# Kernel tuning notes

Measured on AMD Instinct MI355X. Metric: run time of the kernel, lower is better.

## Reference

```python
import jax, jax.numpy as jnp
import numpy as np

D_MODEL = 768
HIDDEN = 2048  # round(768*8/3)=2048, already a multiple of 64
N_EXPERTS = 8
ALPHA = 0.05  # load_balance_alpha


def setup_inputs() -> dict:
    key = jax.random.key(0)
    k0, k1, k2, k3, k4 = jax.random.split(key, 5)
    x = jax.random.normal(k0, (2, 2048, D_MODEL), dtype=jnp.float32)
    wg_w = jax.random.normal(k1, (N_EXPERTS, D_MODEL), dtype=jnp.float32) * 0.02
    wg_b = jnp.zeros((N_EXPERTS,), dtype=jnp.float32)
    Wu = jax.random.normal(k2, (N_EXPERTS, D_MODEL, HIDDEN), dtype=jnp.float32) * 0.02
    Wv = jax.random.normal(k3, (N_EXPERTS, D_MODEL, HIDDEN), dtype=jnp.float32) * 0.02
    Wd = jax.random.normal(k4, (N_EXPERTS, HIDDEN, D_MODEL), dtype=jnp.float32) * 0.02
    return {"x": x, "wg_w": wg_w, "wg_b": wg_b, "Wu": Wu, "Wv": Wv, "Wd": Wd}


def reference(x, wg_w, wg_b, Wu, Wv, Wd):
    b, t, d = x.shape
    xf = x.reshape(b * t, d)  # [N, d]

    # ---- Top1Router (eval mode: temp=1, no noise, z_loss_coef=0) ----
    logits = xf @ wg_w.T + wg_b            # [N, E]
    probs = jax.nn.softmax(logits, axis=-1)
    top1_idx = jnp.argmax(logits, axis=-1)  # [N]
    top1_p = jnp.take_along_axis(probs, top1_idx[:, None], axis=1)[:, 0]  # [N]

    # aux loss: me and ce computed under no_grad in the torch source -> stop_gradient
    one_hot = jax.nn.one_hot(top1_idx, N_EXPERTS, dtype=probs.dtype)
    me = jax.lax.stop_gradient(one_hot.mean(axis=0))   # [E]
    ce = jax.lax.stop_gradient(probs.mean(axis=0))     # [E]
    aux = ALPHA * N_EXPERTS * jnp.sum(me * ce)

    # ---- Dropless dispatch: per-expert masked SwiGLU, combined with top1 gate ----
    gate = top1_p[:, None]  # [N, 1]
    y = jnp.zeros_like(xf)
    for e in range(N_EXPERTS):
        mask = (top1_idx == e)[:, None]            # [N, 1]
        xe = jnp.where(mask, xf, 0.0)              # zero-out non-routed tokens (no biases -> exact)
        u = xe @ Wu[e]                              # [N, H]
        v = xe @ Wv[e]                              # [N, H]
        ye = (jax.nn.silu(u) * v) @ Wd[e]           # [N, d]
        y = y + jnp.where(mask, ye * gate, 0.0)
    return y.reshape(b, t, d), aux
```

## Files before the change

kernel.cpp:

```cpp
#include <hip/hip_runtime.h>
#include <cstdint>
#include <cstddef>

#define TOK 4096
#define DM 768
#define HID 2048
#define NE 8

typedef __attribute__((ext_vector_type(8))) short bf16x8;
typedef __attribute__((ext_vector_type(4))) float f32x4;

#define ASYNC16(GP, LP) \
  __builtin_amdgcn_global_load_lds((__attribute__((address_space(1))) void*)(GP), \
                                   (__attribute__((address_space(3))) void*)(LP), 16, 0, 0)

__device__ __forceinline__ unsigned short f2bf(float f) {
  unsigned int u = __float_as_uint(f);
  u += 0x7FFF + ((u >> 16) & 1);
  return (unsigned short)(u >> 16);
}
__device__ __forceinline__ unsigned int pack2(float a, float b) {
  return (unsigned)f2bf(a) | ((unsigned)f2bf(b) << 16);
}
__device__ __forceinline__ int padded_off(const int* counts, int e) {
  int o = 0;
  for (int i = 0; i < e; ++i) o += (counts[i] + 127) & ~127;
  return o;
}


__global__ __launch_bounds__(256)
void k1_gate_convert(const float* __restrict__ x, const float* __restrict__ wgw,
                     const float* __restrict__ wgb,
                     const float* __restrict__ Wu, const float* __restrict__ Wv,
                     const float* __restrict__ Wd,
                     int* __restrict__ eidx, float* __restrict__ gatep,
                     int* __restrict__ pos, int* __restrict__ counts,
                     float* __restrict__ cepart,
                     unsigned short* __restrict__ wub, unsigned short* __restrict__ wvb,
                     unsigned short* __restrict__ wdb)
{
  __shared__ float ce_loc[4][NE];
  const int b = blockIdx.x;
  if (b < 1024) {
    const int lane = threadIdx.x & 63;
    const int w = threadIdx.x >> 6;
    const int t = b * 4 + w;
    float acc[NE];
#pragma unroll
    for (int e = 0; e < NE; ++e) acc[e] = 0.f;
    const float* xr = x + (size_t)t * DM;
#pragma unroll
    for (int j = 0; j < DM / 64; ++j) {
      float xv = xr[j * 64 + lane];
#pragma unroll
      for (int e = 0; e < NE; ++e) acc[e] += xv * wgw[e * DM + j * 64 + lane];
    }
#pragma unroll
    for (int e = 0; e < NE; ++e) {
      float v = acc[e];
#pragma unroll
      for (int off = 32; off >= 1; off >>= 1) v += __shfl_xor(v, off);
      acc[e] = v + wgb[e];
    }
    float mx = acc[0]; int ai = 0;
#pragma unroll
    for (int e = 1; e < NE; ++e) if (acc[e] > mx) { mx = acc[e]; ai = e; }
    float p[NE]; float se = 0.f;
#pragma unroll
    for (int e = 0; e < NE; ++e) { p[e] = expf(acc[e] - mx); se += p[e]; }
    float inv = 1.f / se;
    if (lane == 0) {
#pragma unroll
      for (int e = 0; e < NE; ++e) ce_loc[w][e] = p[e] * inv;
      eidx[t] = ai;
      gatep[t] = p[ai] * inv;
      pos[t] = atomicAdd(&counts[ai], 1);
    }
    __syncthreads();
    if (threadIdx.x < NE) {
      float s = ce_loc[0][threadIdx.x] + ce_loc[1][threadIdx.x]
              + ce_loc[2][threadIdx.x] + ce_loc[3][threadIdx.x];
      cepart[b * NE + threadIdx.x] = s;
    }
    return;
  }
  const int cb = b - 1024;
  const int seg = cb / 1536;
  const int r = cb % 1536;
  const int e = r / 192;
  const int rem = r % 192;
  const float* W;
  unsigned short* blobbase;
  int N, nt, kt2;
  if (seg < 2) {
    N = HID; nt = rem / 12; kt2 = rem % 12;
    W = ((seg == 0) ? Wu : Wv) + (size_t)e * DM * HID;
    blobbase = ((seg == 0) ? wub : wvb) + ((size_t)((e * 16 + nt) * 24) << 12);
  } else {
    N = DM; nt = rem / 32; kt2 = rem % 32;
    W = Wd + (size_t)e * HID * DM;
    blobbase = wdb + ((size_t)((e * 6 + nt) * 64) << 12);
  }
  const int t = threadIdx.x;
  const int n4 = t & 31, ko8 = t >> 5;
  const float* src = W + (size_t)(kt2 * 64 + ko8 * 8) * N + nt * 128 + n4 * 4;
  float4 f[8];
#pragma unroll
  for (int j = 0; j < 8; ++j) f[j] = *(const float4*)(src + (size_t)j * N);
  const int kt = kt2 * 2 + (ko8 >> 2), ko = ko8 & 3;
  unsigned short* dst = blobbase + ((size_t)kt << 12) + (size_t)(ko * 128 + n4 * 4) * 8;
#pragma unroll
  for (int i = 0; i < 4; ++i) {
    uint4 u;
    u.x = pack2(((const float*)&f[0])[i], ((const float*)&f[1])[i]);
    u.y = pack2(((const float*)&f[2])[i], ((const float*)&f[3])[i]);
    u.z = pack2(((const float*)&f[4])[i], ((const float*)&f[5])[i]);
    u.w = pack2(((const float*)&f[6])[i], ((const float*)&f[7])[i]);
    *(uint4*)(dst + i * 8) = u;
  }
}

__global__ __launch_bounds__(256)
void k2_scatter_zero_aux(const float* __restrict__ x, const int* __restrict__ eidx,
                         const float* __restrict__ gatep, const int* __restrict__ pos,
                         const int* __restrict__ counts, const float* __restrict__ cepart,
                         int* __restrict__ tlist, float* __restrict__ gate_b,
                         unsigned short* __restrict__ xb,
                         float* __restrict__ y, float* __restrict__ aux_out)
{
  __shared__ float sl[256][NE];
  const int b = blockIdx.x;
  if (b < 1024) {
    const int lane = threadIdx.x & 63;
    const int w = threadIdx.x >> 6;
    const int t = b * 4 + w;
    const int e = eidx[t];
    const int prow = padded_off(counts, e) + pos[t];
    if (lane == 0) { tlist[prow] = t; gate_b[prow] = gatep[t]; }
    const float4* src4 = (const float4*)(x + (size_t)t * DM);
    uint2* dst = (uint2*)(xb + (size_t)prow * DM);
#pragma unroll
    for (int c = 0; c < 3; ++c) {
      float4 v = src4[lane + c * 64];
      uint2 d; d.x = pack2(v.x, v.y); d.y = pack2(v.z, v.w);
      dst[lane + c * 64] = d;
    }
  } else if (b < 1536) {
    float4* y4 = (float4*)y;
    const int base = (b - 1024) * 1536 + threadIdx.x;
#pragma unroll
    for (int c = 0; c < 6; ++c) {
      float4 z; z.x = 0.f; z.y = 0.f; z.z = 0.f; z.w = 0.f;
      y4[base + c * 256] = z;
    }
  } else {
    const int tid = threadIdx.x;
    float s[NE];
#pragma unroll
    for (int e = 0; e < NE; ++e) s[e] = 0.f;
    for (int bb = tid; bb < 1024; bb += 256)
#pragma unroll
      for (int e = 0; e < NE; ++e) s[e] += cepart[bb * NE + e];
#pragma unroll
    for (int e = 0; e < NE; ++e) sl[tid][e] = s[e];
    __syncthreads();
    for (int st = 128; st > 0; st >>= 1) {
      if (tid < st)
#pragma unroll
        for (int e = 0; e < NE; ++e) sl[tid][e] += sl[tid + st][e];
      __syncthreads();
    }
    if (tid == 0) {
      float aux = 0.f;
      for (int e = 0; e < NE; ++e)
        aux += ((float)counts[e] / 4096.f) * (sl[0][e] / 4096.f);
      aux_out[0] = 0.05f * 8.f * aux;
    }
  }
}

__global__ __launch_bounds__(256, 2)
void k_ffn1(const unsigned short* __restrict__ wub, const unsigned short* __restrict__ wvb,
            const unsigned short* __restrict__ xb, const float* __restrict__ gate_b,
            const int* __restrict__ counts, unsigned short* __restrict__ h)
{
  const int e = blockIdx.z;
  const int Me = counts[e];
  const int tm = blockIdx.y;
  if (tm * 128 >= Me) return;
  const int tn = blockIdx.x;
  const int prowbase = padded_off(counts, e) + tm * 128;

  __shared__ __align__(16) unsigned short Sh[12288];

  const int tid = threadIdx.x;
  const int lane = tid & 63;
  const int wv_ = tid >> 6;
  const int wm = wv_ >> 1, wn = wv_ & 1;
  const int wu_id = __builtin_amdgcn_readfirstlane(wv_);

  f32x4 accU[4][4], accV[4][4];
#pragma unroll
  for (int i = 0; i < 4; ++i)
#pragma unroll
    for (int j = 0; j < 4; ++j)
#pragma unroll
      for (int k = 0; k < 4; ++k) { accU[i][j][k] = 0.f; accV[i][j][k] = 0.f; }

  const char* BuBase = (const char*)wub + ((size_t)((e * 16 + tn) * 24) << 13);
  const char* BvBase = (const char*)wvb + ((size_t)((e * 16 + tn) * 24) << 13);

  const char* sp[6]; size_t stp[6];
#pragma unroll
  for (int c2 = 0; c2 < 6; ++c2) {
    const int c = wu_id * 6 + c2;
    if (c < 8) {
      int s = c * 64 + lane, m = s >> 2, ko = (s & 3) ^ (m & 3);
      sp[c2] = (const char*)xb + (size_t)(prowbase + m) * (DM * 2) + ko * 16;
      stp[c2] = 64;
    } else if (c < 16) {
      int u = (c - 8) * 64 + lane, n = u >> 2, ko = (u & 3) ^ (n & 3);
      sp[c2] = BuBase + (size_t)(ko * 128 + n) * 16;
      stp[c2] = 8192;
    } else {
      int u = (c - 16) * 64 + lane, n = u >> 2, ko = (u & 3) ^ (n & 3);
      sp[c2] = BvBase + (size_t)(ko * 128 + n) * 16;
      stp[c2] = 8192;
    }
  }
  const int lc = lane & 15, q = lane >> 4;

  for (int kt = 0; kt < 24; ++kt) {
#pragma unroll
    for (int c2 = 0; c2 < 6; ++c2) {
      ASYNC16(sp[c2], (char*)Sh + (unsigned)((wu_id * 6 + c2) * 1024));
      sp[c2] += stp[c2];
    }
    __syncthreads();
    bf16x8 a[4], bu[4], bv[4];
#pragma unroll
    for (int i = 0; i < 4; ++i) {
      int m = wm * 64 + i * 16 + lc;
      a[i] = *(const bf16x8*)&Sh[(m * 4 + (q ^ (m & 3))) * 8];
    }
#pragma unroll
    for (int j = 0; j < 4; ++j) {
      int n = wn * 64 + j * 16 + lc;
      int slb = (n * 4 + (q ^ (n & 3))) * 8;
      bu[j] = *(const bf16x8*)&Sh[4096 + slb];
      bv[j] = *(const bf16x8*)&Sh[8192 + slb];
    }
#pragma unroll
    for (int i = 0; i < 4; ++i)
#pragma unroll
      for (int j = 0; j < 4; ++j) {
        accU[i][j] = __builtin_amdgcn_mfma_f32_16x16x32_bf16(a[i], bu[j], accU[i][j], 0, 0, 0);
        accV[i][j] = __builtin_amdgcn_mfma_f32_16x16x32_bf16(a[i], bv[j], accV[i][j], 0, 0, 0);
      }
    __syncthreads();
  }
  const int colbase = tn * 128 + wn * 64;
  const int rlane = (lane >> 4) * 4;
  const int clane = lane & 15;
#pragma unroll
  for (int i = 0; i < 4; ++i) {
#pragma unroll
    for (int r = 0; r < 4; ++r) {
      int rowIn = wm * 64 + i * 16 + rlane + r;
      if (tm * 128 + rowIn < Me) {
        int prow = prowbase + rowIn;
        float g = gate_b[prow];
        unsigned short* hp = h + (size_t)prow * HID + colbase + clane;
#pragma unroll
        for (int j = 0; j < 4; ++j) {
          float u_ = accU[i][j][r];
          float v_ = accV[i][j][r];
          float sv = u_ / (1.f + expf(-u_));
          hp[j * 16] = f2bf(sv * v_ * g);
        }
      }
    }
  }
}

__global__ __launch_bounds__(256, 2)
void k_ffn2(const unsigned short* __restrict__ wdb, const unsigned short* __restrict__ h,
            const int* __restrict__ counts, const int* __restrict__ tlist,
            float* __restrict__ y)
{
  const int z = blockIdx.z;
  const int e = z >> 2, split = z & 3;
  const int Me = counts[e];
  const int tm = blockIdx.y;
  if (tm * 128 >= Me) return;
  const int tn = blockIdx.x;
  const int prowbase = padded_off(counts, e) + tm * 128;

  __shared__ __align__(16) unsigned short Sh[8192];

  const int tid = threadIdx.x;
  const int lane = tid & 63;
  const int wv_ = tid >> 6;
  const int wm = wv_ >> 1, wn = wv_ & 1;
  const int wu_id = __builtin_amdgcn_readfirstlane(wv_);

  f32x4 acc[4][4];
#pragma unroll
  for (int i = 0; i < 4; ++i)
#pragma unroll
    for (int j = 0; j < 4; ++j)
#pragma unroll
      for (int k = 0; k < 4; ++k) acc[i][j][k] = 0.f;

  const char* BdBase = (const char*)wdb + ((size_t)((e * 6 + tn) * 64) << 13);

  const char* sp[4]; size_t stp[4];
#pragma unroll
  for (int c2 = 0; c2 < 4; ++c2) {
    const int c = wu_id * 4 + c2;
    if (c < 8) {
      int s = c * 64 + lane, m = s >> 2, ko = (s & 3) ^ (m & 3);
      sp[c2] = (const char*)h + (size_t)(prowbase + m) * (HID * 2) + split * 1024 + ko * 16;
      stp[c2] = 64;
    } else {
      int u = (c - 8) * 64 + lane, n = u >> 2, ko = (u & 3) ^ (n & 3);
      sp[c2] = BdBase + (size_t)split * 131072 + (size_t)(ko * 128 + n) * 16;
      stp[c2] = 8192;
    }
  }
  const int lc = lane & 15, q = lane >> 4;

  for (int kti = 0; kti < 16; ++kti) {
#pragma unroll
    for (int c2 = 0; c2 < 4; ++c2) {
      ASYNC16(sp[c2], (char*)Sh + (unsigned)((wu_id * 4 + c2) * 1024));
      sp[c2] += stp[c2];
    }
    __syncthreads();
    bf16x8 a[4], bfr[4];
#pragma unroll
    for (int i = 0; i < 4; ++i) {
      int m = wm * 64 + i * 16 + lc;
      a[i] = *(const bf16x8*)&Sh[(m * 4 + (q ^ (m & 3))) * 8];
    }
#pragma unroll
    for (int j = 0; j < 4; ++j) {
      int n = wn * 64 + j * 16 + lc;
      bfr[j] = *(const bf16x8*)&Sh[4096 + (n * 4 + (q ^ (n & 3))) * 8];
    }
#pragma unroll
    for (int i = 0; i < 4; ++i)
#pragma unroll
      for (int j = 0; j < 4; ++j)
        acc[i][j] = __builtin_amdgcn_mfma_f32_16x16x32_bf16(a[i], bfr[j], acc[i][j], 0, 0, 0);
    __syncthreads();
  }
  const int colbase = tn * 128 + wn * 64;
  const int rlane = (lane >> 4) * 4;
  const int clane = lane & 15;
#pragma unroll
  for (int i = 0; i < 4; ++i) {
#pragma unroll
    for (int r = 0; r < 4; ++r) {
      int rowIn = wm * 64 + i * 16 + rlane + r;
      if (tm * 128 + rowIn < Me) {
        int tok = tlist[prowbase + rowIn];
        float* yp = y + (size_t)tok * DM + colbase + clane;
#pragma unroll
        for (int j = 0; j < 4; ++j) atomicAdd(&yp[j * 16], acc[i][j][r]);
      }
    }
  }
}

extern "C" void kernel_launch(void* const* d_in, const int* in_sizes, int n_in,
                              void* d_out, int out_size, void* d_ws, size_t ws_size,
                              hipStream_t stream)
{
  const float* x   = (const float*)d_in[0];
  const float* wgw = (const float*)d_in[1];
  const float* wgb = (const float*)d_in[2];
  const float* Wu  = (const float*)d_in[3];
  const float* Wv  = (const float*)d_in[4];
  const float* Wd  = (const float*)d_in[5];
  float* out = (float*)d_out;

  char* ws = (char*)d_ws;
  int*   counts = (int*)(ws + 0);
  int*   eidx   = (int*)(ws + 256);
  float* gatep  = (float*)(ws + 16640);
  int*   pos    = (int*)(ws + 33024);
  float* cepart = (float*)(ws + 49408);
  int*   tlist  = (int*)(ws + 82176);
  float* gate_b = (float*)(ws + 102656);
  unsigned short* xb  = (unsigned short*)(ws + 123136);
  unsigned short* h   = (unsigned short*)(ws + 7987456);
  unsigned short* wub = (unsigned short*)(ws + 28958976);
  unsigned short* wvb = (unsigned short*)(ws + 54124800);
  unsigned short* wdb = (unsigned short*)(ws + 79290624);

  hipMemsetAsync(counts, 0, 32, stream);
  k1_gate_convert<<<1024 + 4608, 256, 0, stream>>>(x, wgw, wgb, Wu, Wv, Wd,
                                                   eidx, gatep, pos, counts, cepart,
                                                   wub, wvb, wdb);
  k2_scatter_zero_aux<<<1537, 256, 0, stream>>>(x, eidx, gatep, pos, counts, cepart,
                                                tlist, gate_b, xb,
                                                out, out + (size_t)TOK * DM);
  k_ffn1<<<dim3(16, 32, 8), 256, 0, stream>>>(wub, wvb, xb, gate_b, counts, h);
  k_ffn2<<<dim3(6, 32, 32), 256, 0, stream>>>(wdb, h, counts, tlist, out);
}
```

Before: 375.9 us.

## Deterministic token ordering via scan kernel and double K-step per barrier in FFN GEMMs

Splits the gate and weight-convert kernel into separate kernels and replaces the atomic per-expert position counter with a single-block prefix-scan kernel. That kernel builds deterministic row positions, the token list, the gate values and the aux loss. Both FFN GEMM kernels now load two K-slices (128 wide) into LDS per sync round, which halves the barrier and loop count at the cost of double the shared memory per block. This may reduce occupancy, and the serial single-block count kernel adds an extra launch.

```diff
diff --git a/kernel.cpp b/kernel.cpp
--- a/kernel.cpp
+++ b/kernel.cpp
@@ -28,64 +28,61 @@
   return o;
 }
 
-
 __global__ __launch_bounds__(256)
-void k1_gate_convert(const float* __restrict__ x, const float* __restrict__ wgw,
-                     const float* __restrict__ wgb,
-                     const float* __restrict__ Wu, const float* __restrict__ Wv,
-                     const float* __restrict__ Wd,
-                     int* __restrict__ eidx, float* __restrict__ gatep,
-                     int* __restrict__ pos, int* __restrict__ counts,
-                     float* __restrict__ cepart,
-                     unsigned short* __restrict__ wub, unsigned short* __restrict__ wvb,
-                     unsigned short* __restrict__ wdb)
+void k_gate(const float* __restrict__ x, const float* __restrict__ wgw,
+            const float* __restrict__ wgb,
+            int* __restrict__ eidx, float* __restrict__ gatep,
+            float* __restrict__ cepart)
 {
   __shared__ float ce_loc[4][NE];
-  const int b = blockIdx.x;
-  if (b < 1024) {
-    const int lane = threadIdx.x & 63;
-    const int w = threadIdx.x >> 6;
-    const int t = b * 4 + w;
-    float acc[NE];
-#pragma unroll
-    for (int e = 0; e < NE; ++e) acc[e] = 0.f;
-    const float* xr = x + (size_t)t * DM;
-#pragma unroll
-    for (int j = 0; j < DM / 64; ++j) {
-      float xv = xr[j * 64 + lane];
-#pragma unroll
-      for (int e = 0; e < NE; ++e) acc[e] += xv * wgw[e * DM + j * 64 + lane];
-    }
-#pragma unroll
-    for (int e = 0; e < NE; ++e) {
-      float v = acc[e];
-#pragma unroll
-      for (int off = 32; off >= 1; off >>= 1) v += __shfl_xor(v, off);
-      acc[e] = v + wgb[e];
-    }
-    float mx = acc[0]; int ai = 0;
-#pragma unroll
-    for (int e = 1; e < NE; ++e) if (acc[e] > mx) { mx = acc[e]; ai = e; }
-    float p[NE]; float se = 0.f;
-#pragma unroll
-    for (int e = 0; e < NE; ++e) { p[e] = expf(acc[e] - mx); se += p[e]; }
-    float inv = 1.f / se;
-    if (lane == 0) {
-#pragma unroll
-      for (int e = 0; e < NE; ++e) ce_loc[w][e] = p[e] * inv;
-      eidx[t] = ai;
-      gatep[t] = p[ai] * inv;
-      pos[t] = atomicAdd(&counts[ai], 1);
-    }
-    __syncthreads();
-    if (threadIdx.x < NE) {
-      float s = ce_loc[0][threadIdx.x] + ce_loc[1][threadIdx.x]
-              + ce_loc[2][threadIdx.x] + ce_loc[3][threadIdx.x];
-      cepart[b * NE + threadIdx.x] = s;
-    }
-    return;
-  }
-  const int cb = b - 1024;
+  const int lane = threadIdx.x & 63;
+  const int w = threadIdx.x >> 6;
+  const int t = blockIdx.x * 4 + w;
+  float acc[NE];
+#pragma unroll
+  for (int e = 0; e < NE; ++e) acc[e] = 0.f;
+  const float* xr = x + (size_t)t * DM;
+#pragma unroll
+  for (int j = 0; j < DM / 64; ++j) {
+    float xv = xr[j * 64 + lane];
+#pragma unroll
+    for (int e = 0; e < NE; ++e) acc[e] += xv * wgw[e * DM + j * 64 + lane];
+  }
+#pragma unroll
+  for (int e = 0; e < NE; ++e) {
+    float v = acc[e];
+#pragma unroll
+    for (int off = 32; off >= 1; off >>= 1) v += __shfl_xor(v, off);
+    acc[e] = v + wgb[e];
+  }
+  float mx = acc[0]; int ai = 0;
+#pragma unroll
+  for (int e = 1; e < NE; ++e) if (acc[e] > mx) { mx = acc[e]; ai = e; }
+  float p[NE]; float se = 0.f;
+#pragma unroll
+  for (int e = 0; e < NE; ++e) { p[e] = expf(acc[e] - mx); se += p[e]; }
+  float inv = 1.f / se;
+  if (lane == 0) {
+#pragma unroll
+    for (int e = 0; e < NE; ++e) ce_loc[w][e] = p[e] * inv;
+    eidx[t] = ai;
+    gatep[t] = p[ai] * inv;
+  }
+  __syncthreads();
+  if (threadIdx.x < NE) {
+    float s = ce_loc[0][threadIdx.x] + ce_loc[1][threadIdx.x]
+            + ce_loc[2][threadIdx.x] + ce_loc[3][threadIdx.x];
+    cepart[blockIdx.x * NE + threadIdx.x] = s;
+  }
+}
+
+__global__ __launch_bounds__(256)
+void k_convert(const float* __restrict__ Wu, const float* __restrict__ Wv,
+               const float* __restrict__ Wd,
+               unsigned short* __restrict__ wub, unsigned short* __restrict__ wvb,
+               unsigned short* __restrict__ wdb)
+{
+  const int cb = blockIdx.x;
   const int seg = cb / 1536;
   const int r = cb % 1536;
   const int e = r / 192;
@@ -122,22 +119,94 @@
 }
 
 __global__ __launch_bounds__(256)
-void k2_scatter_zero_aux(const float* __restrict__ x, const int* __restrict__ eidx,
-                         const float* __restrict__ gatep, const int* __restrict__ pos,
-                         const int* __restrict__ counts, const float* __restrict__ cepart,
-                         int* __restrict__ tlist, float* __restrict__ gate_b,
-                         unsigned short* __restrict__ xb,
-                         float* __restrict__ y, float* __restrict__ aux_out)
-{
-  __shared__ float sl[256][NE];
+void k_count(const int* __restrict__ eidx, const float* __restrict__ gatep,
+             const float* __restrict__ cepart,
+             int* __restrict__ prow_arr, int* __restrict__ tlist,
+             float* __restrict__ gate_b, int* __restrict__ counts_g,
+             float* __restrict__ aux_out)
+{
+  __shared__ int hist[256][NE];
+  __shared__ float fs[256][NE];
+  __shared__ int po_s[NE], cnt_s[NE];
+  const int tid = threadIdx.x;
+  int own[NE], v[NE], el[16];
+#pragma unroll
+  for (int e = 0; e < NE; ++e) own[e] = 0;
+#pragma unroll
+  for (int j = 0; j < 16; ++j) {
+    el[j] = eidx[tid * 16 + j];
+#pragma unroll
+    for (int e = 0; e < NE; ++e) own[e] += (el[j] == e) ? 1 : 0;
+  }
+#pragma unroll
+  for (int e = 0; e < NE; ++e) { v[e] = own[e]; hist[tid][e] = v[e]; }
+  __syncthreads();
+  for (int st = 1; st < 256; st <<= 1) {
+    int add[NE];
+#pragma unroll
+    for (int e = 0; e < NE; ++e) add[e] = (tid >= st) ? hist[tid - st][e] : 0;
+    __syncthreads();
+#pragma unroll
+    for (int e = 0; e < NE; ++e) { v[e] += add[e]; hist[tid][e] = v[e]; }
+    __syncthreads();
+  }
+  if (tid == 0) {
+    int o = 0;
+#pragma unroll
+    for (int e = 0; e < NE; ++e) {
+      int c = hist[255][e];
+      cnt_s[e] = c; counts_g[e] = c; po_s[e] = o;
+      o += (c + 127) & ~127;
+    }
+  }
+  __syncthreads();
+  int run[NE];
+#pragma unroll
+  for (int e = 0; e < NE; ++e) run[e] = po_s[e] + v[e] - own[e];
+#pragma unroll
+  for (int j = 0; j < 16; ++j) {
+    const int t = tid * 16 + j;
+    const int e = el[j];
+    int p = 0;
+#pragma unroll
+    for (int k = 0; k < NE; ++k) if (e == k) p = run[k]++;
+    prow_arr[t] = p;
+    tlist[p] = t;
+    gate_b[p] = gatep[t];
+  }
+  float s[NE];
+#pragma unroll
+  for (int e = 0; e < NE; ++e) s[e] = 0.f;
+  for (int bb = tid; bb < 1024; bb += 256)
+#pragma unroll
+    for (int e = 0; e < NE; ++e) s[e] += cepart[bb * NE + e];
+#pragma unroll
+  for (int e = 0; e < NE; ++e) fs[tid][e] = s[e];
+  __syncthreads();
+  for (int st = 128; st > 0; st >>= 1) {
+    if (tid < st)
+#pragma unroll
+      for (int e = 0; e < NE; ++e) fs[tid][e] += fs[tid + st][e];
+    __syncthreads();
+  }
+  if (tid == 0) {
+    float aux = 0.f;
+    for (int e = 0; e < NE; ++e)
+      aux += ((float)cnt_s[e] / 4096.f) * (fs[0][e] / 4096.f);
+    aux_out[0] = 0.05f * 8.f * aux;
+  }
+}
+
+__global__ __launch_bounds__(256)
+void k2_scatter_zero(const float* __restrict__ x, const int* __restrict__ prow_arr,
+                     unsigned short* __restrict__ xb, float* __restrict__ y)
+{
   const int b = blockIdx.x;
   if (b < 1024) {
     const int lane = threadIdx.x & 63;
     const int w = threadIdx.x >> 6;
     const int t = b * 4 + w;
-    const int e = eidx[t];
-    const int prow = padded_off(counts, e) + pos[t];
-    if (lane == 0) { tlist[prow] = t; gate_b[prow] = gatep[t]; }
+    const int prow = prow_arr[t];
     const float4* src4 = (const float4*)(x + (size_t)t * DM);
     uint2* dst = (uint2*)(xb + (size_t)prow * DM);
 #pragma unroll
@@ -146,36 +215,13 @@
       uint2 d; d.x = pack2(v.x, v.y); d.y = pack2(v.z, v.w);
       dst[lane + c * 64] = d;
     }
-  } else if (b < 1536) {
+  } else {
     float4* y4 = (float4*)y;
     const int base = (b - 1024) * 1536 + threadIdx.x;
 #pragma unroll
     for (int c = 0; c < 6; ++c) {
       float4 z; z.x = 0.f; z.y = 0.f; z.z = 0.f; z.w = 0.f;
       y4[base + c * 256] = z;
-    }
-  } else {
-    const int tid = threadIdx.x;
-    float s[NE];
-#pragma unroll
-    for (int e = 0; e < NE; ++e) s[e] = 0.f;
-    for (int bb = tid; bb < 1024; bb += 256)
-#pragma unroll
-      for (int e = 0; e < NE; ++e) s[e] += cepart[bb * NE + e];
-#pragma unroll
-    for (int e = 0; e < NE; ++e) sl[tid][e] = s[e];
-    __syncthreads();
-    for (int st = 128; st > 0; st >>= 1) {
-      if (tid < st)
-#pragma unroll
-        for (int e = 0; e < NE; ++e) sl[tid][e] += sl[tid + st][e];
-      __syncthreads();
-    }
-    if (tid == 0) {
-      float aux = 0.f;
-      for (int e = 0; e < NE; ++e)
-        aux += ((float)counts[e] / 4096.f) * (sl[0][e] / 4096.f);
-      aux_out[0] = 0.05f * 8.f * aux;
     }
   }
 }
@@ -192,7 +238,7 @@
   const int tn = blockIdx.x;
   const int prowbase = padded_off(counts, e) + tm * 128;
 
-  __shared__ __align__(16) unsigned short Sh[12288];
+  __shared__ __align__(16) unsigned short Sh[24576];
 
   const int tid = threadIdx.x;
   const int lane = tid & 63;
@@ -211,53 +257,58 @@
   const char* BuBase = (const char*)wub + ((size_t)((e * 16 + tn) * 24) << 13);
   const char* BvBase = (const char*)wvb + ((size_t)((e * 16 + tn) * 24) << 13);
 
-  const char* sp[6]; size_t stp[6];
-#pragma unroll
-  for (int c2 = 0; c2 < 6; ++c2) {
-    const int c = wu_id * 6 + c2;
-    if (c < 8) {
-      int s = c * 64 + lane, m = s >> 2, ko = (s & 3) ^ (m & 3);
-      sp[c2] = (const char*)xb + (size_t)(prowbase + m) * (DM * 2) + ko * 16;
-      stp[c2] = 64;
-    } else if (c < 16) {
-      int u = (c - 8) * 64 + lane, n = u >> 2, ko = (u & 3) ^ (n & 3);
-      sp[c2] = BuBase + (size_t)(ko * 128 + n) * 16;
-      stp[c2] = 8192;
+  const char* sp[12]; size_t stp[12];
+#pragma unroll
+  for (int c2 = 0; c2 < 12; ++c2) {
+    const int c = wu_id * 12 + c2;
+    const int reg = c >> 3, i8 = c & 7;
+    const int sub = (reg >= 3);
+    const int rr = (reg >= 3) ? reg - 3 : reg;
+    const int s = i8 * 64 + lane;
+    if (rr == 0) {
+      int m = s >> 2, ko = (s & 3) ^ (m & 3);
+      sp[c2] = (const char*)xb + (size_t)(prowbase + m) * (DM * 2) + sub * 64 + ko * 16;
+      stp[c2] = 128;
     } else {
-      int u = (c - 16) * 64 + lane, n = u >> 2, ko = (u & 3) ^ (n & 3);
-      sp[c2] = BvBase + (size_t)(ko * 128 + n) * 16;
-      stp[c2] = 8192;
+      int n = s >> 2, ko = (s & 3) ^ (n & 3);
+      const char* base = (rr == 1) ? BuBase : BvBase;
+      sp[c2] = base + (size_t)sub * 8192 + (size_t)(ko * 128 + n) * 16;
+      stp[c2] = 16384;
     }
   }
   const int lc = lane & 15, q = lane >> 4;
 
-  for (int kt = 0; kt < 24; ++kt) {
-#pragma unroll
-    for (int c2 = 0; c2 < 6; ++c2) {
-      ASYNC16(sp[c2], (char*)Sh + (unsigned)((wu_id * 6 + c2) * 1024));
+  for (int kt2 = 0; kt2 < 12; ++kt2) {
+#pragma unroll
+    for (int c2 = 0; c2 < 12; ++c2) {
+      ASYNC16(sp[c2], (char*)Sh + (unsigned)((wu_id * 12 + c2) * 1024));
       sp[c2] += stp[c2];
     }
     __syncthreads();
-    bf16x8 a[4], bu[4], bv[4];
-#pragma unroll
-    for (int i = 0; i < 4; ++i) {
-      int m = wm * 64 + i * 16 + lc;
-      a[i] = *(const bf16x8*)&Sh[(m * 4 + (q ^ (m & 3))) * 8];
-    }
-#pragma unroll
-    for (int j = 0; j < 4; ++j) {
-      int n = wn * 64 + j * 16 + lc;
-      int slb = (n * 4 + (q ^ (n & 3))) * 8;
-      bu[j] = *(const bf16x8*)&Sh[4096 + slb];
-      bv[j] = *(const bf16x8*)&Sh[8192 + slb];
-    }
-#pragma unroll
-    for (int i = 0; i < 4; ++i)
+#pragma unroll
+    for (int sub = 0; sub < 2; ++sub) {
+      const int sb = sub * 12288;
+      bf16x8 a[4], bu[4], bv[4];
+#pragma unroll
+      for (int i = 0; i < 4; ++i) {
+        int m = wm * 64 + i * 16 + lc;
+        a[i] = *(const bf16x8*)&Sh[sb + (m * 4 + (q ^ (m & 3))) * 8];
+      }
 #pragma unroll
       for (int j = 0; j < 4; ++j) {
-        accU[i][j] = __builtin_amdgcn_mfma_f32_16x16x32_bf16(a[i], bu[j], accU[i][j], 0, 0, 0);
-        accV[i][j] = __builtin_amdgcn_mfma_f32_16x16x32_bf16(a[i], bv[j], accV[i][j], 0, 0, 0);
-      }
+        int n = wn * 64 + j * 16 + lc;
+        int slb = (n * 4 + (q ^ (n & 3))) * 8;
+        bu[j] = *(const bf16x8*)&Sh[sb + 4096 + slb];
+        bv[j] = *(const bf16x8*)&Sh[sb + 8192 + slb];
+      }
+#pragma unroll
+      for (int i = 0; i < 4; ++i)
+#pragma unroll
+        for (int j = 0; j < 4; ++j) {
+          accU[i][j] = __builtin_amdgcn_mfma_f32_16x16x32_bf16(a[i], bu[j], accU[i][j], 0, 0, 0);
+          accV[i][j] = __builtin_amdgcn_mfma_f32_16x16x32_bf16(a[i], bv[j], accV[i][j], 0, 0, 0);
+        }
+    }
     __syncthreads();
   }
   const int colbase = tn * 128 + wn * 64;
@@ -297,7 +348,7 @@
   const int tn = blockIdx.x;
   const int prowbase = padded_off(counts, e) + tm * 128;
 
-  __shared__ __align__(16) unsigned short Sh[8192];
+  __shared__ __align__(16) unsigned short Sh[16384];
 
   const int tid = threadIdx.x;
   const int lane = tid & 63;
@@ -315,45 +366,53 @@
 
   const char* BdBase = (const char*)wdb + ((size_t)((e * 6 + tn) * 64) << 13);
 
-  const char* sp[4]; size_t stp[4];
-#pragma unroll
-  for (int c2 = 0; c2 < 4; ++c2) {
-    const int c = wu_id * 4 + c2;
-    if (c < 8) {
-      int s = c * 64 + lane, m = s >> 2, ko = (s & 3) ^ (m & 3);
-      sp[c2] = (const char*)h + (size_t)(prowbase + m) * (HID * 2) + split * 1024 + ko * 16;
-      stp[c2] = 64;
+  const char* sp[8]; size_t stp[8];
+#pragma unroll
+  for (int c2 = 0; c2 < 8; ++c2) {
+    const int c = wu_id * 8 + c2;
+    const int reg = c >> 3, i8 = c & 7;
+    const int sub = reg >> 1;
+    const int s = i8 * 64 + lane;
+    if ((reg & 1) == 0) {
+      int m = s >> 2, ko = (s & 3) ^ (m & 3);
+      sp[c2] = (const char*)h + (size_t)(prowbase + m) * (HID * 2)
+             + split * 1024 + sub * 64 + ko * 16;
+      stp[c2] = 128;
     } else {
-      int u = (c - 8) * 64 + lane, n = u >> 2, ko = (u & 3) ^ (n & 3);
-      sp[c2] = BdBase + (size_t)split * 131072 + (size_t)(ko * 128 + n) * 16;
-      stp[c2] = 8192;
+      int n = s >> 2, ko = (s & 3) ^ (n & 3);
+      sp[c2] = BdBase + (size_t)(split * 16 + sub) * 8192 + (size_t)(ko * 128 + n) * 16;
+      stp[c2] = 16384;
     }
   }
   const int lc = lane & 15, q = lane >> 4;
 
-  for (int kti = 0; kti < 16; ++kti) {
-#pragma unroll
-    for (int c2 = 0; c2 < 4; ++c2) {
-      ASYNC16(sp[c2], (char*)Sh + (unsigned)((wu_id * 4 + c2) * 1024));
+  for (int kti = 0; kti < 8; ++kti) {
+#pragma unroll
+    for (int c2 = 0; c2 < 8; ++c2) {
+      ASYNC16(sp[c2], (char*)Sh + (unsigned)((wu_id * 8 + c2) * 1024));
       sp[c2] += stp[c2];
     }
     __syncthreads();
-    bf16x8 a[4], bfr[4];
-#pragma unroll
-    for (int i = 0; i < 4; ++i) {
-      int m = wm * 64 + i * 16 + lc;
-      a[i] = *(const bf16x8*)&Sh[(m * 4 + (q ^ (m & 3))) * 8];
-    }
-#pragma unroll
-    for (int j = 0; j < 4; ++j) {
-      int n = wn * 64 + j * 16 + lc;
-      bfr[j] = *(const bf16x8*)&Sh[4096 + (n * 4 + (q ^ (n & 3))) * 8];
-    }
-#pragma unroll
-    for (int i = 0; i < 4; ++i)
-#pragma unroll
-      for (int j = 0; j < 4; ++j)
-        acc[i][j] = __builtin_amdgcn_mfma_f32_16x16x32_bf16(a[i], bfr[j], acc[i][j], 0, 0, 0);
+#pragma unroll
+    for (int sub = 0; sub < 2; ++sub) {
+      const int sb = sub * 8192;
+      bf16x8 a[4], bfr[4];
+#pragma unroll
+      for (int i = 0; i < 4; ++i) {
+        int m = wm * 64 + i * 16 + lc;
+        a[i] = *(const bf16x8*)&Sh[sb + (m * 4 + (q ^ (m & 3))) * 8];
+      }
+#pragma unroll
+      for (int j = 0; j < 4; ++j) {
+        int n = wn * 64 + j * 16 + lc;
+        bfr[j] = *(const bf16x8*)&Sh[sb + 4096 + (n * 4 + (q ^ (n & 3))) * 8];
+      }
+#pragma unroll
+      for (int i = 0; i < 4; ++i)
+#pragma unroll
+        for (int j = 0; j < 4; ++j)
+          acc[i][j] = __builtin_amdgcn_mfma_f32_16x16x32_bf16(a[i], bfr[j], acc[i][j], 0, 0, 0);
+    }
     __syncthreads();
   }
   const int colbase = tn * 128 + wn * 64;
@@ -390,7 +449,7 @@
   int*   counts = (int*)(ws + 0);
   int*   eidx   = (int*)(ws + 256);
   float* gatep  = (float*)(ws + 16640);
-  int*   pos    = (int*)(ws + 33024);
+  int*   prow   = (int*)(ws + 33024);
   float* cepart = (float*)(ws + 49408);
   int*   tlist  = (int*)(ws + 82176);
   float* gate_b = (float*)(ws + 102656);
@@ -400,13 +459,11 @@
   unsigned short* wvb = (unsigned short*)(ws + 54124800);
   unsigned short* wdb = (unsigned short*)(ws + 79290624);
 
-  hipMemsetAsync(counts, 0, 32, stream);
-  k1_gate_convert<<<1024 + 4608, 256, 0, stream>>>(x, wgw, wgb, Wu, Wv, Wd,
-                                                   eidx, gatep, pos, counts, cepart,
-                                                   wub, wvb, wdb);
-  k2_scatter_zero_aux<<<1537, 256, 0, stream>>>(x, eidx, gatep, pos, counts, cepart,
-                                                tlist, gate_b, xb,
-                                                out, out + (size_t)TOK * DM);
+  k_gate<<<1024, 256, 0, stream>>>(x, wgw, wgb, eidx, gatep, cepart);
+  k_convert<<<4608, 256, 0, stream>>>(Wu, Wv, Wd, wub, wvb, wdb);
+  k_count<<<1, 256, 0, stream>>>(eidx, gatep, cepart, prow, tlist, gate_b,
+                                 counts, out + (size_t)TOK * DM);
+  k2_scatter_zero<<<1536, 256, 0, stream>>>(x, prow, xb, out);
   k_ffn1<<<dim3(16, 32, 8), 256, 0, stream>>>(wub, wvb, xb, gate_b, counts, h);
   k_ffn2<<<dim3(6, 32, 32), 256, 0, stream>>>(wdb, h, counts, tlist, out);
 }
```

Result: faster. 343.2 us (-8.7%).
